# Performance work log

Measured on AMD Instinct MI355X. Metric: run time of the kernel, lower is better.

Reference implementation:

```python
import jax, jax.numpy as jnp
import numpy as np

S, B, D, H = 1024, 16, 512, 8
DH = D // H  # 64


def setup_inputs() -> dict:
    key = jax.random.key(0)
    k1, k2, k3, k4, k5 = jax.random.split(key, 5)
    x = jax.random.normal(k1, (S, B, D), dtype=jnp.float32)
    # binary validity mask [B, S]: 1 = keep, 0 = masked out (matches torch usage)
    mask = (jax.random.uniform(k2, (B, S)) > 0.2).astype(jnp.float32)
    scale = 1.0 / np.sqrt(D)
    wq = jax.random.normal(k3, (H, DH, D), dtype=jnp.float32) * scale
    wk = jax.random.normal(k4, (H, DH, D), dtype=jnp.float32) * scale
    wv = jax.random.normal(k5, (H, DH, D), dtype=jnp.float32) * scale
    return {"x": x, "mask": mask, "wq": wq, "wk": wk, "wv": wv}


def reference(x, mask, wq, wk, wv):
    # x: [S, B, D]; mask: [B, S]; w*: [H, DH, D] (stacked bias-free Linear weights)
    dh = wq.shape[1]
    # per-hop projections for all hops at once (Linear: y = x @ W.T)
    q = jnp.einsum('sbd,hed->bhse', x, wq)  # [B,H,S,DH]
    k = jnp.einsum('sbd,hed->bhse', x, wk)
    v = jnp.einsum('sbd,hed->bhse', x, wv)
    scores = jnp.einsum('bhse,bhte->bhst', q, k)  # [B,H,S,S]
    inv_mask = (1.0 - mask)[:, None, None, :]      # broadcast over heads, query pos
    align = jnp.tanh(scores / jnp.sqrt(jnp.asarray(dh, x.dtype))) - 10000.0 * inv_mask
    align = jax.nn.softmax(align, axis=-1)
    out = jnp.einsum('bhst,bhte->bhse', align, v)  # [B,H,S,DH]
    s, b = x.shape[0], x.shape[1]
    # concat hops along feature dim, back to seq-first: [S, B, H*DH]
    return jnp.transpose(out, (2, 0, 1, 3)).reshape(s, b, -1)
```

## Files before the change

kernel.cpp:

```cpp
#include <hip/hip_runtime.h>
#include <stdint.h>
#include <stddef.h>

#define SS 1024
#define BB 16
#define DD 512
#define HH 8
#define DHH 64

typedef __attribute__((ext_vector_type(8))) short bf16x8;
typedef __attribute__((ext_vector_type(4))) float f32x4;
typedef __attribute__((ext_vector_type(16))) float f32x16;
typedef __attribute__((ext_vector_type(4))) float float4v;
typedef __attribute__((ext_vector_type(4))) unsigned short us4;
typedef __attribute__((ext_vector_type(4))) unsigned int uint4v;

__device__ __forceinline__ unsigned short f2bf(float f) {
  union { float f; unsigned int u; } v; v.f = f;
  unsigned int x = v.u;
  return (unsigned short)((x + 0x7FFFu + ((x >> 16) & 1u)) >> 16);
}

#define GLDS16(dst, src)                                                                  \
  __builtin_amdgcn_global_load_lds(                                                      \
      (const __attribute__((address_space(1))) unsigned int*)(const void*)(src),         \
      (__attribute__((address_space(3))) unsigned int*)(void*)(dst), 16, 0, 0)

__global__ void cvt_kernel(const float* __restrict__ x,
                           const float* __restrict__ wq,
                           const float* __restrict__ wk,
                           const float* __restrict__ wv,
                           unsigned short* __restrict__ xb,
                           unsigned short* __restrict__ wb) {
  const int i = blockIdx.x * 256 + threadIdx.x;
  const int n_x4 = (SS * BB * DD) / 4;
  if (i < n_x4) {
    float4v v = ((const float4v*)x)[i];
    us4 o;
    o[0] = f2bf(v[0]); o[1] = f2bf(v[1]); o[2] = f2bf(v[2]); o[3] = f2bf(v[3]);
    ((us4*)xb)[i] = o;
  } else {
    const int j = i - n_x4;
    const int sel = j >> 16;
    const int off4 = j & 65535;
    const float* wsrc = (sel == 0) ? wq : ((sel == 1) ? wk : wv);
    const float scale = (sel == 0) ? 0.36067376022224085f : 1.0f;
    float4v v = ((const float4v*)wsrc)[off4];
    us4 o;
    o[0] = f2bf(v[0] * scale); o[1] = f2bf(v[1] * scale);
    o[2] = f2bf(v[2] * scale); o[3] = f2bf(v[3] * scale);
    ((us4*)wb)[(sel << 16) + off4] = o;
  }
}

__global__ __launch_bounds__(256) void proj_kernel(
    const unsigned short* __restrict__ xb,
    const unsigned short* __restrict__ wb,
    unsigned short* __restrict__ qb,
    unsigned short* __restrict__ kb,
    unsigned short* __restrict__ vt) {
  const int bm = blockIdx.x * 128;
  const int bn = blockIdx.y * 128;
  const int b = blockIdx.z / 3;
  const int wsel = blockIdx.z % 3;

  __shared__ unsigned short At[128 * 32];
  __shared__ unsigned short Bt[128 * 32];
  __shared__ unsigned short OT[4][64 * 72];

  const int tid = threadIdx.x;
  const int w = tid >> 6;
  const int lane = tid & 63;

  const unsigned short* wptr = wb + wsel * (512 * DD);

  f32x4 acc[4][4];
#pragma unroll
  for (int mi = 0; mi < 4; ++mi)
#pragma unroll
    for (int ni = 0; ni < 4; ++ni) acc[mi][ni] = (f32x4){0.f, 0.f, 0.f, 0.f};

  const int m0 = (w & 1) * 64;
  const int n0 = (w >> 1) * 64;

  for (int kt = 0; kt < 16; ++kt) {
#pragma unroll
    for (int i = 0; i < 2; ++i) {
      const int idx8 = i * 256 + tid;
      const int r = idx8 >> 2;
      const int c8 = idx8 & 3;
      GLDS16(&At[(i * 256 + w * 64) * 8],
             xb + (size_t)(bm + r) * (BB * DD) + b * DD + kt * 32 + c8 * 8);
      GLDS16(&Bt[(i * 256 + w * 64) * 8],
             wptr + (size_t)(bn + r) * DD + kt * 32 + c8 * 8);
    }
    __syncthreads();
    bf16x8 af[4], bfr[4];
#pragma unroll
    for (int mi = 0; mi < 4; ++mi)
      af[mi] = *(const bf16x8*)&At[(m0 + mi * 16 + (lane & 15)) * 32 + (lane >> 4) * 8];
#pragma unroll
    for (int ni = 0; ni < 4; ++ni)
      bfr[ni] = *(const bf16x8*)&Bt[(n0 + ni * 16 + (lane & 15)) * 32 + (lane >> 4) * 8];
#pragma unroll
    for (int mi = 0; mi < 4; ++mi)
#pragma unroll
      for (int ni = 0; ni < 4; ++ni)
        acc[mi][ni] =
            __builtin_amdgcn_mfma_f32_16x16x32_bf16(af[mi], bfr[ni], acc[mi][ni], 0, 0, 0);
    __syncthreads();
  }

  const int h = (bn + n0) >> 6;
  unsigned short* OTw = &OT[w][0];
  if (wsel != 2) {
#pragma unroll
    for (int mi = 0; mi < 4; ++mi)
#pragma unroll
      for (int ni = 0; ni < 4; ++ni)
#pragma unroll
        for (int j = 0; j < 4; ++j)
          OTw[(mi * 16 + (lane >> 4) * 4 + j) * 72 + ni * 16 + (lane & 15)] =
              f2bf(acc[mi][ni][j]);
  } else {
#pragma unroll
    for (int mi = 0; mi < 4; ++mi)
#pragma unroll
      for (int ni = 0; ni < 4; ++ni) {
        us4 pk;
#pragma unroll
        for (int j = 0; j < 4; ++j) pk[j] = f2bf(acc[mi][ni][j]);
        *(us4*)&OTw[(ni * 16 + (lane & 15)) * 72 + mi * 16 + (lane >> 4) * 4] = pk;
      }
  }
  unsigned short* gout = (wsel == 0) ? qb : ((wsel == 1) ? kb : vt);
#pragma unroll
  for (int pass = 0; pass < 8; ++pass) {
    const int row = pass * 8 + (lane >> 3);
    bf16x8 vrow = *(const bf16x8*)&OTw[row * 72 + (lane & 7) * 8];
    size_t dst;
    if (wsel != 2)
      dst = ((size_t)(b * HH + h) * SS + (size_t)(bm + m0 + row)) * DHH + (lane & 7) * 8;
    else
      dst = ((size_t)(b * HH + h) * DHH + (size_t)row) * SS + (bm + m0) + (lane & 7) * 8;
    *(bf16x8*)&gout[dst] = vrow;
  }
}

__global__ __launch_bounds__(256, 4) void attn_kernel(
    const unsigned short* __restrict__ qb,
    const unsigned short* __restrict__ kb,
    const unsigned short* __restrict__ vt,
    const float* __restrict__ mask,
    float* __restrict__ out) {
  const int id = blockIdx.x;
  const int xcd = id & 7;
  const int slot = id >> 3;
  const int bh = xcd * 16 + (slot >> 3);
  const int qt = slot & 7;
  const int b = bh >> 3;
  const int h = bh & 7;
  const int tid = threadIdx.x;
  const int w = tid >> 6;
  const int lane = tid & 63;
  const int l31 = lane & 31;
  const int hi32 = lane >> 5;
  const int sl = (l31 & 0x13) | ((l31 & 4) << 1) | ((l31 & 8) >> 1);

  __shared__ unsigned short Ks[2][64 * 64];
  __shared__ unsigned short Vs[2][64 * 64];
  __shared__ float rs_s[4][32];

  const size_t base_qk = (size_t)bh * SS * DHH;
  const int q0 = qt * 128 + w * 32;

  bf16x8 aq[4];
  {
    const unsigned short* qp = qb + base_qk + (size_t)(q0 + l31) * DHH + hi32 * 8;
    aq[0] = *(const bf16x8*)(qp);
    aq[1] = *(const bf16x8*)(qp + 16);
    aq[2] = *(const bf16x8*)(qp + 32);
    aq[3] = *(const bf16x8*)(qp + 48);
  }

  const int srow = w * 16 + (lane >> 3);
  const unsigned short* kg = kb + base_qk + (size_t)srow * DHH + (lane & 7) * 8;
  const unsigned short* vg =
      vt + (size_t)bh * DHH * SS + (size_t)srow * SS + (lane & 7) * 8;
  const int lofs = srow * 128 + (((lane & 7) ^ (lane >> 3)) << 4);

  f32x16 accO[2];
#pragma unroll
  for (int n = 0; n < 2; ++n)
#pragma unroll
    for (int i = 0; i < 16; ++i) accO[n][i] = 0.f;
  float rs = 0.f;
  const float* mrow = mask + b * SS;

  {
    uint4v a0 = *(const uint4v*)kg;
    uint4v a1 = *(const uint4v*)(kg + 8 * DHH);
    uint4v a2 = *(const uint4v*)vg;
    uint4v a3 = *(const uint4v*)(vg + 8 * SS);
    *(uint4v*)((char*)&Ks[0][0] + lofs) = a0;
    *(uint4v*)((char*)&Ks[0][0] + lofs + 1024) = a1;
    *(uint4v*)((char*)&Vs[0][0] + lofs) = a2;
    *(uint4v*)((char*)&Vs[0][0] + lofs + 1024) = a3;
  }
  __syncthreads();

  int buf = 0;
  for (int kt = 0; kt < 16; ++kt) {
    uint4v nk0, nk1, nv0, nv1;
    if (kt < 15) {
      const unsigned short* kgn = kg + (size_t)(kt + 1) * (64 * DHH);
      const unsigned short* vgn = vg + (size_t)(kt + 1) * 64;
      nk0 = *(const uint4v*)kgn;
      nk1 = *(const uint4v*)(kgn + 8 * DHH);
      nv0 = *(const uint4v*)vgn;
      nv1 = *(const uint4v*)(vgn + 8 * SS);
    }
    const char* Kb = (const char*)&Ks[buf][0];
    const char* Vb = (const char*)&Vs[buf][0];

#pragma unroll
    for (int T = 0; T < 2; ++T) {
      const int krow = T * 32 + sl;
      const int ksw = (krow & 7) << 4;
      f32x16 sc = {};
      __builtin_amdgcn_s_setprio(1);
#pragma unroll
      for (int ks = 0; ks < 4; ++ks) {
        bf16x8 kf = *(const bf16x8*)(Kb + krow * 128 + ((ks * 32 + hi32 * 16) ^ ksw));
        sc = __builtin_amdgcn_mfma_f32_32x32x16_bf16(kf, aq[ks], sc, 0, 0, 0);
      }
      __builtin_amdgcn_s_setprio(0);
      unsigned int pu[16];
#pragma unroll
      for (int g = 0; g < 4; ++g) {
        float4v mv = *(const float4v*)&mrow[kt * 64 + T * 32 + (g >> 1) * 16 +
                                            hi32 * 8 + (g & 1) * 4];
        float u0 = __builtin_fminf(__builtin_amdgcn_exp2f(sc[g * 4 + 0]), 16384.f);
        float u1 = __builtin_fminf(__builtin_amdgcn_exp2f(sc[g * 4 + 1]), 16384.f);
        float u2 = __builtin_fminf(__builtin_amdgcn_exp2f(sc[g * 4 + 2]), 16384.f);
        float u3 = __builtin_fminf(__builtin_amdgcn_exp2f(sc[g * 4 + 3]), 16384.f);
        float n0 = __builtin_fmaf(__builtin_fmaf(19.f, u0, 22.f), u0, 7.f);
        float n1 = __builtin_fmaf(__builtin_fmaf(19.f, u1, 22.f), u1, 7.f);
        float n2 = __builtin_fmaf(__builtin_fmaf(19.f, u2, 22.f), u2, 7.f);
        float n3 = __builtin_fmaf(__builtin_fmaf(19.f, u3, 22.f), u3, 7.f);
        float d0 = __builtin_fmaf(__builtin_fmaf(7.f, u0, 22.f), u0, 19.f);
        float d1 = __builtin_fmaf(__builtin_fmaf(7.f, u1, 22.f), u1, 19.f);
        float d2 = __builtin_fmaf(__builtin_fmaf(7.f, u2, 22.f), u2, 19.f);
        float d3 = __builtin_fmaf(__builtin_fmaf(7.f, u3, 22.f), u3, 19.f);
        float p01 = d0 * d1, p23 = d2 * d3;
        float rq = __builtin_amdgcn_rcpf(p01 * p23);
        float r01 = p23 * rq, r23 = p01 * rq;
        float qr0 = d1 * r01, qr1 = d0 * r01, qr2 = d3 * r23, qr3 = d2 * r23;
        float p0 = (mv[0] * n0) * qr0;
        float p1 = (mv[1] * n1) * qr1;
        float p2 = (mv[2] * n2) * qr2;
        float p3 = (mv[3] * n3) * qr3;
        rs += p0; rs += p1; rs += p2; rs += p3;
        union { float f; unsigned int u; } c0, c1, c2, c3;
        c0.f = p0; c1.f = p1; c2.f = p2; c3.f = p3;
        pu[g * 4 + 0] = c0.u; pu[g * 4 + 1] = c1.u;
        pu[g * 4 + 2] = c2.u; pu[g * 4 + 3] = c3.u;
      }
      union { unsigned int u[4]; bf16x8 v; } f0, f1;
#pragma unroll
      for (int m = 0; m < 4; ++m) {
        f0.u[m] = __builtin_amdgcn_perm(pu[2 * m + 1], pu[2 * m], 0x07060302u);
        f1.u[m] = __builtin_amdgcn_perm(pu[8 + 2 * m + 1], pu[8 + 2 * m], 0x07060302u);
      }
      __builtin_amdgcn_s_setprio(1);
#pragma unroll
      for (int n = 0; n < 2; ++n) {
        const int vrow = n * 32 + l31;
        const int vsw = (vrow & 7) << 4;
        bf16x8 bv0 = *(const bf16x8*)(Vb + vrow * 128 + (((T * 2 + 0) * 32 + hi32 * 16) ^ vsw));
        bf16x8 bv1 = *(const bf16x8*)(Vb + vrow * 128 + (((T * 2 + 1) * 32 + hi32 * 16) ^ vsw));
        accO[n] = __builtin_amdgcn_mfma_f32_32x32x16_bf16(f0.v, bv0, accO[n], 0, 0, 0);
        accO[n] = __builtin_amdgcn_mfma_f32_32x32x16_bf16(f1.v, bv1, accO[n], 0, 0, 0);
      }
      __builtin_amdgcn_s_setprio(0);
    }

    if (kt < 15) {
      char* Kn = (char*)&Ks[buf ^ 1][0];
      char* Vn = (char*)&Vs[buf ^ 1][0];
      *(uint4v*)(Kn + lofs) = nk0;
      *(uint4v*)(Kn + lofs + 1024) = nk1;
      *(uint4v*)(Vn + lofs) = nv0;
      *(uint4v*)(Vn + lofs + 1024) = nv1;
    }
    __syncthreads();
    buf ^= 1;
  }

  rs += __shfl_xor(rs, 32, 64);
  if (hi32 == 0) rs_s[w][l31] = __builtin_amdgcn_rcpf(rs);
  float4v ri[4];
#pragma unroll
  for (int g = 0; g < 4; ++g) ri[g] = *(const float4v*)&rs_s[w][g * 8 + hi32 * 4];

#pragma unroll
  for (int n = 0; n < 2; ++n)
#pragma unroll
    for (int g = 0; g < 4; ++g)
#pragma unroll
      for (int i = 0; i < 4; ++i) {
        const int qrow = q0 + g * 8 + hi32 * 4 + i;
        out[((size_t)qrow * BB + b) * DD + h * DHH + n * 32 + l31] =
            accO[n][g * 4 + i] * ri[g][i];
      }
}

extern "C" void kernel_launch(void* const* d_in, const int* in_sizes, int n_in,
                              void* d_out, int out_size, void* d_ws, size_t ws_size,
                              hipStream_t stream) {
  const float* x = (const float*)d_in[0];
  const float* mask = (const float*)d_in[1];
  const float* wq = (const float*)d_in[2];
  const float* wk = (const float*)d_in[3];
  const float* wv = (const float*)d_in[4];
  float* out = (float*)d_out;

  char* ws = (char*)d_ws;
  unsigned short* xb = (unsigned short*)(ws);
  unsigned short* wb = (unsigned short*)(ws + (16ull << 20));
  unsigned short* qb = (unsigned short*)(ws + (18ull << 20));
  unsigned short* kb = (unsigned short*)(ws + (34ull << 20));
  unsigned short* vt = (unsigned short*)(ws + (50ull << 20));

  cvt_kernel<<<dim3(8960), 256, 0, stream>>>(x, wq, wk, wv, xb, wb);
  proj_kernel<<<dim3(8, 4, 48), 256, 0, stream>>>(xb, wb, qb, kb, vt);
  attn_kernel<<<dim3(1024), 256, 0, stream>>>(qb, kb, vt, mask, out);
}
```

Measured before the change: 133.4 us.

## Stage attention K/V tiles via direct global-to-LDS loads and alias projection shared memory

The attention kernel's double-buffered K/V prefetch now uses global_load_lds (direct global-to-LDS DMA) in place of register loads followed by LDS stores. The XOR swizzle moves onto the global source address so the LDS layout stays the same. This frees VGPRs and removes the separate LDS store instructions. The projection kernel also aliases its A/B staging tiles and output transpose buffers into one shared pool to cut LDS footprint and possibly raise occupancy. There are no explicit vmcnt waits before __syncthreads, so correctness depends on the compiler inserting waits for the async LDS writes.

Measured after the change: 134.5 us. No clear change (+0.8%).

```diff
diff --git a/kernel.cpp b/kernel.cpp
--- a/kernel.cpp
+++ b/kernel.cpp
@@ -13,7 +13,6 @@
 typedef __attribute__((ext_vector_type(16))) float f32x16;
 typedef __attribute__((ext_vector_type(4))) float float4v;
 typedef __attribute__((ext_vector_type(4))) unsigned short us4;
-typedef __attribute__((ext_vector_type(4))) unsigned int uint4v;
 
 __device__ __forceinline__ unsigned short f2bf(float f) {
   union { float f; unsigned int u; } v; v.f = f;
@@ -64,9 +63,9 @@
   const int b = blockIdx.z / 3;
   const int wsel = blockIdx.z % 3;
 
-  __shared__ unsigned short At[128 * 32];
-  __shared__ unsigned short Bt[128 * 32];
-  __shared__ unsigned short OT[4][64 * 72];
+  __shared__ unsigned short pool[4 * 64 * 72];
+  unsigned short* At = pool;
+  unsigned short* Bt = pool + 4096;
 
   const int tid = threadIdx.x;
   const int w = tid >> 6;
@@ -112,7 +111,7 @@
   }
 
   const int h = (bn + n0) >> 6;
-  unsigned short* OTw = &OT[w][0];
+  unsigned short* OTw = pool + w * 4608;
   if (wsel != 2) {
 #pragma unroll
     for (int mi = 0; mi < 4; ++mi)
@@ -183,11 +182,23 @@
     aq[3] = *(const bf16x8*)(qp + 48);
   }
 
-  const int srow = w * 16 + (lane >> 3);
-  const unsigned short* kg = kb + base_qk + (size_t)srow * DHH + (lane & 7) * 8;
-  const unsigned short* vg =
-      vt + (size_t)bh * DHH * SS + (size_t)srow * SS + (lane & 7) * 8;
-  const int lofs = srow * 128 + (((lane & 7) ^ (lane >> 3)) << 4);
+  const int sr0 = w * 16 + (lane >> 3);
+  const int sxb = (((lane & 7) ^ (lane >> 3)) << 4);
+  const unsigned short* ksrc0 = kb + base_qk + (size_t)sr0 * DHH + (sxb >> 1);
+  const unsigned short* ksrc1 = ksrc0 + 8 * DHH;
+  const unsigned short* vsrc0 =
+      vt + (size_t)bh * DHH * SS + (size_t)sr0 * SS + (sxb >> 1);
+  const unsigned short* vsrc1 = vsrc0 + 8 * SS;
+
+#define STAGE(bb, kt2)                                                       \
+  do {                                                                       \
+    GLDS16(&Ks[bb][(w * 16) * 64], ksrc0 + (size_t)(kt2) * (64 * DHH));      \
+    GLDS16(&Ks[bb][(w * 16 + 8) * 64], ksrc1 + (size_t)(kt2) * (64 * DHH));  \
+    GLDS16(&Vs[bb][(w * 16) * 64], vsrc0 + (size_t)(kt2) * 64);              \
+    GLDS16(&Vs[bb][(w * 16 + 8) * 64], vsrc1 + (size_t)(kt2) * 64);          \
+  } while (0)
+
+  STAGE(0, 0);
 
   f32x16 accO[2];
 #pragma unroll
@@ -197,29 +208,11 @@
   float rs = 0.f;
   const float* mrow = mask + b * SS;
 
-  {
-    uint4v a0 = *(const uint4v*)kg;
-    uint4v a1 = *(const uint4v*)(kg + 8 * DHH);
-    uint4v a2 = *(const uint4v*)vg;
-    uint4v a3 = *(const uint4v*)(vg + 8 * SS);
-    *(uint4v*)((char*)&Ks[0][0] + lofs) = a0;
-    *(uint4v*)((char*)&Ks[0][0] + lofs + 1024) = a1;
-    *(uint4v*)((char*)&Vs[0][0] + lofs) = a2;
-    *(uint4v*)((char*)&Vs[0][0] + lofs + 1024) = a3;
-  }
   __syncthreads();
 
   int buf = 0;
   for (int kt = 0; kt < 16; ++kt) {
-    uint4v nk0, nk1, nv0, nv1;
-    if (kt < 15) {
-      const unsigned short* kgn = kg + (size_t)(kt + 1) * (64 * DHH);
-      const unsigned short* vgn = vg + (size_t)(kt + 1) * 64;
-      nk0 = *(const uint4v*)kgn;
-      nk1 = *(const uint4v*)(kgn + 8 * DHH);
-      nv0 = *(const uint4v*)vgn;
-      nv1 = *(const uint4v*)(vgn + 8 * SS);
-    }
+    if (kt < 15) STAGE(buf ^ 1, kt + 1);
     const char* Kb = (const char*)&Ks[buf][0];
     const char* Vb = (const char*)&Vs[buf][0];
 
@@ -284,18 +277,10 @@
       }
       __builtin_amdgcn_s_setprio(0);
     }
-
-    if (kt < 15) {
-      char* Kn = (char*)&Ks[buf ^ 1][0];
-      char* Vn = (char*)&Vs[buf ^ 1][0];
-      *(uint4v*)(Kn + lofs) = nk0;
-      *(uint4v*)(Kn + lofs + 1024) = nk1;
-      *(uint4v*)(Vn + lofs) = nv0;
-      *(uint4v*)(Vn + lofs + 1024) = nv1;
-    }
     __syncthreads();
     buf ^= 1;
   }
+#undef STAGE
 
   rs += __shfl_xor(rs, 32, 64);
   if (hi32 == 0) rs_s[w][l31] = __builtin_amdgcn_rcpf(rs);
```
